# Optimization experiments

Measured on AMD Instinct MI355X. Metric: run time of the kernel, lower is better.

## Reference

```python
import jax, jax.numpy as jnp
import numpy as np

K = 8
TEMP = 0.05
EPS = 1e-8


def setup_inputs() -> dict:
    key = jax.random.key(0)
    k1, k2, k3, k4, k5, k6 = jax.random.split(key, 6)
    N, D, H = 8192, 1024, 64
    h0 = jax.random.normal(k1, (N, D), dtype=jnp.float32)
    coords = jax.random.uniform(k2, (N, 2), dtype=jnp.float32)
    # tiny MLP params: Linear(2,H) -> ReLU -> Linear(H,1) -> Sigmoid
    W1 = jax.random.normal(k3, (2, H), dtype=jnp.float32) * (1.0 / np.sqrt(2))
    b1 = jnp.zeros((H,), dtype=jnp.float32)
    W2 = jax.random.normal(k4, (H, 1), dtype=jnp.float32) * (1.0 / np.sqrt(H))
    b2 = jnp.zeros((1,), dtype=jnp.float32)
    return {"h0": h0, "coords": coords, "W1": W1, "b1": b1, "W2": W2, "b2": b2}


def reference(h0, coords, W1, b1, W2, b2):
    # pairwise euclidean distances [N, N]
    sq = jnp.sum(coords * coords, axis=-1)                      # [N]
    d2 = sq[:, None] + sq[None, :] - 2.0 * (coords @ coords.T)  # [N, N]
    dist = jnp.sqrt(jnp.maximum(d2, 0.0))

    # k+1 nearest (smallest dist), drop self (index 0)
    _, idx = jax.lax.top_k(-dist, K + 1)                        # [N, K+1]
    knn_idx = idx[:, 1:]                                        # [N, K]

    # gather neighbor features [N, K, D]
    neighbor_feats = h0[knn_idx]

    # cosine similarity between h_i and each neighbor (torch eps semantics)
    num = jnp.einsum('nd,nkd->nk', h0, neighbor_feats)          # [N, K]
    ni = jnp.maximum(jnp.linalg.norm(h0, axis=-1), EPS)         # [N]
    nj = jnp.maximum(jnp.linalg.norm(neighbor_feats, axis=-1), EPS)  # [N, K]
    sim = num / (ni[:, None] * nj)

    # spatial weights from gathered distances
    d_knn = jnp.take_along_axis(dist, knn_idx, axis=1)          # [N, K]
    spatial_w = jnp.exp(-d_knn / TEMP)

    density_input = jnp.stack(
        [sim.mean(axis=1), spatial_w.mean(axis=1)], axis=1)     # [N, 2]

    hmid = jax.nn.relu(density_input @ W1 + b1)
    density = jax.nn.sigmoid(hmid @ W2 + b2)                    # [N, 1]
    return density
```

## Files before the change

### kernel.cpp

```cpp
#include <hip/hip_runtime.h>
#include <math.h>

#define NROWS 8192
#define DIM   1024
#define GRID  64
#define CELLW 0.015625f
#define LPR   16

__device__ __forceinline__ int cell_of(float v) {
    int c = (int)(v * 64.0f);
    return c < 0 ? 0 : (c > 63 ? 63 : c);
}

__device__ __forceinline__ float np_d2(float xi, float yi, float sqi,
                                       float xj, float yj) {
    float sqj = __fadd_rn(__fmul_rn(xj, xj), __fmul_rn(yj, yj));
    float G   = fmaf(yi, yj, __fmul_rn(xi, xj));
    return __fsub_rn(__fadd_rn(sqi, sqj), __fmul_rn(2.0f, G));
}

__global__ __launch_bounds__(1024) void build_grid_kernel(
    const float* __restrict__ coords,
    int* __restrict__ cellStart,
    float4* __restrict__ sxyz) {

    __shared__ int lcnt[4096];
    __shared__ int wsum[16];
    const int t = threadIdx.x;

    for (int i = t; i < 4096; i += 1024) lcnt[i] = 0;
    __syncthreads();

    float2 pc[8]; int pcell[8];
#pragma unroll
    for (int k = 0; k < 8; ++k) {
        int i = t + 1024 * k;
        float2 c = ((const float2*)coords)[i];
        pc[k] = c;
        pcell[k] = cell_of(c.y) * GRID + cell_of(c.x);
        atomicAdd(&lcnt[pcell[k]], 1);
    }
    __syncthreads();

    int c0 = lcnt[t*4+0], c1 = lcnt[t*4+1], c2 = lcnt[t*4+2], c3 = lcnt[t*4+3];
    int s1 = c0, s2 = c0 + c1, s3 = s2 + c2, s4 = s3 + c3;
    int lane = t & 63, wid = t >> 6;
    int inc = s4;
#pragma unroll
    for (int off = 1; off < 64; off <<= 1) {
        int o = __shfl_up(inc, off, 64);
        if (lane >= off) inc += o;
    }
    if (lane == 63) wsum[wid] = inc;
    __syncthreads();
    int wbase = 0;
    for (int w = 0; w < wid; ++w) wbase += wsum[w];
    int excl = wbase + inc - s4;

    cellStart[t*4+0] = excl;
    cellStart[t*4+1] = excl + s1;
    cellStart[t*4+2] = excl + s2;
    cellStart[t*4+3] = excl + s3;
    if (t == 1023) cellStart[4096] = excl + s4;
    lcnt[t*4+0] = excl;
    lcnt[t*4+1] = excl + s1;
    lcnt[t*4+2] = excl + s2;
    lcnt[t*4+3] = excl + s3;
    __syncthreads();

#pragma unroll
    for (int k = 0; k < 8; ++k) {
        int pos = atomicAdd(&lcnt[pcell[k]], 1);
        float x = pc[k].x, y = pc[k].y;
        float sq = __fadd_rn(__fmul_rn(x, x), __fmul_rn(y, y));
        sxyz[pos] = make_float4(x, y, sq, __int_as_float(t + 1024 * k));
    }
}

__global__ __launch_bounds__(256) void knn_kernel(
    const int* __restrict__ cellStart,
    const float4* __restrict__ sxyz,
    unsigned long long* __restrict__ chosen_ws) {

    const int sub = threadIdx.x & (LPR - 1);
    const int g   = (blockIdx.x * 256 + threadIdx.x) / LPR;

    const float4 me = sxyz[g];
    const float xi = me.x, yi = me.y, sqi = me.z;
    const int row = __float_as_int(me.w);
    const int cx = cell_of(xi), cy = cell_of(yi);

    unsigned long long best[10], merged[10];
    int C = 2;
    while (true) {
#pragma unroll
        for (int s = 0; s < 10; ++s) best[s] = ~0ULL;
        int x0 = max(0, cx - C), x1 = min(GRID - 1, cx + C);
        int y0 = max(0, cy - C), y1 = min(GRID - 1, cy + C);
        for (int yy = y0; yy <= y1; ++yy) {
            int s = cellStart[yy * GRID + x0];
            int e = cellStart[yy * GRID + x1 + 1];
            for (int t = s + sub; t < e; t += LPR) {
                float4 c = sxyz[t];
                float d2  = __fsub_rn(__fadd_rn(sqi, c.z),
                                      __fmul_rn(2.0f, fmaf(yi, c.y, __fmul_rn(xi, c.x))));
                float dst = __fsqrt_rn(fmaxf(d2, 0.0f));
                unsigned long long key =
                    ((unsigned long long)__float_as_uint(dst) << 32)
                    | (unsigned int)__float_as_int(c.w);
                if (key < best[9]) {
                    best[9] = key;
#pragma unroll
                    for (int ss = 9; ss >= 1; --ss) {
                        unsigned long long a = best[ss - 1], b = best[ss];
                        unsigned long long lo = a < b ? a : b;
                        unsigned long long hi = a < b ? b : a;
                        best[ss - 1] = lo;
                        best[ss]     = hi;
                    }
                }
            }
        }
#pragma unroll
        for (int r = 0; r < 10; ++r) {
            unsigned long long mn = best[0];
#pragma unroll
            for (int off = 1; off < LPR; off <<= 1) {
                unsigned long long o = __shfl_xor(mn, off, 64);
                mn = (o < mn) ? o : mn;
            }
            if (best[0] == mn) {
#pragma unroll
                for (int ss = 0; ss < 9; ++ss) best[ss] = best[ss + 1];
                best[9] = ~0ULL;
            }
            merged[r] = mn;
        }
        bool done = false;
        if (merged[9] != ~0ULL) {
            float d9 = __uint_as_float((unsigned int)(merged[9] >> 32));
            if (d9 + 1.0e-3f <= (float)C * CELLW) done = true;
        }
        if (done || C >= GRID) break;
        C <<= 1; if (C > GRID) C = GRID;
    }

    if (sub == 0) {
        unsigned long long* o = chosen_ws + (size_t)row * 10;
#pragma unroll
        for (int r = 0; r < 10; ++r) o[r] = merged[r];
    }
}

__global__ __launch_bounds__(256) void gather_final_kernel(
    const float* __restrict__ h0,
    const float* __restrict__ coords,
    const unsigned long long* __restrict__ chosen_ws,
    const float4* __restrict__ sxyz,
    const float* __restrict__ W1, const float* __restrict__ b1,
    const float* __restrict__ W2, const float* __restrict__ b2,
    float* __restrict__ out) {

    __shared__ float2 pq[11];

    const int widx = threadIdx.x >> 6;
    const int lane = threadIdx.x & 63;
    const int bid  = blockIdx.x;
    const int g    = (bid & 7) * (NROWS / 8) + (bid >> 3);
    const int row  = __float_as_int(sxyz[g].w);

    const float4* hi = (const float4*)(h0 + (size_t)row * DIM);
    float4 a[4];
#pragma unroll
    for (int t = 0; t < 4; ++t) a[t] = hi[lane + 64 * t];

    const unsigned long long* ch = chosen_ws + (size_t)row * 10;

    for (int s = widx; s <= 10; s += 4) {
        float p = 0.f, q = 0.f;
        if (s == 10) {
#pragma unroll
            for (int t = 0; t < 4; ++t)
                p += a[t].x * a[t].x + a[t].y * a[t].y + a[t].z * a[t].z + a[t].w * a[t].w;
            q = p;
        } else {
            int j = (int)(ch[s] & 0xFFFFFFFFu);
            const float4* hj = (const float4*)(h0 + (size_t)j * DIM);
#pragma unroll
            for (int t = 0; t < 4; ++t) {
                float4 b = hj[lane + 64 * t];
                p += a[t].x * b.x + a[t].y * b.y + a[t].z * b.z + a[t].w * b.w;
                q += b.x * b.x + b.y * b.y + b.z * b.z + b.w * b.w;
            }
        }
#pragma unroll
        for (int off = 1; off < 64; off <<= 1) {
            p += __shfl_xor(p, off, 64);
            q += __shfl_xor(q, off, 64);
        }
        if (lane == 0) pq[s] = make_float2(p, q);
    }
    __syncthreads();

    if (widx != 0) return;

    const float2 ci = ((const float2*)coords)[row];
    const float xi = ci.x, yi = ci.y;
    const float sqi = __fadd_rn(__fmul_rn(xi, xi), __fmul_rn(yi, yi));

    unsigned long long chosen[10];
#pragma unroll
    for (int r = 0; r < 10; ++r) chosen[r] = ch[r];

    auto clamped_d2 = [&](unsigned long long key) -> float {
        int j = (int)(key & 0xFFFFFFFFu);
        float2 cj = ((const float2*)coords)[j];
        return fmaxf(np_d2(xi, yi, sqi, cj.x, cj.y), 0.0f);
    };
    const float m0 = clamped_d2(chosen[0]);
    const float m1 = clamped_d2(chosen[1]);
    const float m2 = clamped_d2(chosen[2]);
    const float m8 = clamped_d2(chosen[8]);
    const float m9 = clamped_d2(chosen[9]);

    const float WIN = 2.0e-6f;
    const bool fpair = (m1 - m0) <= WIN;
    const bool ftri  = fpair && ((m2 - m0) <= WIN);
    const bool f89   = (m9 - m8) <= WIN;

    float wd[3];
    wd[0] = ftri ? (1.f / 3.f) : (fpair ? 0.5f : 1.0f);
    wd[1] = ftri ? (1.f / 3.f) : (fpair ? 0.5f : 0.0f);
    wd[2] = ftri ? (1.f / 3.f) : 0.0f;
    const float wc0 = f89 ? 0.5f : 1.0f;
    const float wc1 = f89 ? 0.5f : 0.0f;

    const float ni = fmaxf(sqrtf(pq[10].x), 1e-8f);

    float sim[10], sw[10];
#pragma unroll
    for (int r = 0; r < 10; ++r) {
        float dst = __uint_as_float((unsigned int)(chosen[r] >> 32));
        float nj  = fmaxf(sqrtf(pq[r].y), 1e-8f);
        sim[r] = pq[r].x / (ni * nj);
        sw[r]  = expf(__fdiv_rn(-dst, 0.05f));
    }

    float Ssim = 0.f, Ssw = 0.f;
#pragma unroll
    for (int r = 0; r < 9; ++r) { Ssim += sim[r]; Ssw += sw[r]; }

    const float w1a = W1[lane], w1b = W1[64 + lane];
    const float b1l = b1[lane], w2l = W2[lane], b2s = b2[0];

    float outacc = 0.f;
#pragma unroll
    for (int d = 0; d < 3; ++d) {
#pragma unroll
        for (int c = 0; c < 2; ++c) {
            float wgt = wd[d] * (c ? wc1 : wc0);
            float simsum = Ssim - sim[d] + (c ? (sim[9] - sim[8]) : 0.f);
            float swsum  = Ssw  - sw[d]  + (c ? (sw[9]  - sw[8])  : 0.f);
            float di0 = simsum * 0.125f;
            float di1 = swsum  * 0.125f;
            float hm = fmaxf(di0 * w1a + di1 * w1b + b1l, 0.f);
            float v  = hm * w2l;
#pragma unroll
            for (int off = 1; off < 64; off <<= 1) v += __shfl_xor(v, off, 64);
            float z = v + b2s;
            outacc += wgt * (1.f / (1.f + expf(-z)));
        }
    }

    if (lane == 0) out[row] = outacc;
}

extern "C" void kernel_launch(void* const* d_in, const int* in_sizes, int n_in,
                              void* d_out, int out_size, void* d_ws, size_t ws_size,
                              hipStream_t stream) {
    const float* h0     = (const float*)d_in[0];
    const float* coords = (const float*)d_in[1];
    const float* W1     = (const float*)d_in[2];
    const float* b1     = (const float*)d_in[3];
    const float* W2     = (const float*)d_in[4];
    const float* b2     = (const float*)d_in[5];
    float* out = (float*)d_out;

    char* ws = (char*)d_ws;
    unsigned long long* chosen_ws = (unsigned long long*)(ws);
    float4* sxyz      = (float4*)(ws + 1015808);
    int*    cellStart = (int*)(ws + 1146880);

    build_grid_kernel  <<<1, 1024, 0, stream>>>(coords, cellStart, sxyz);
    knn_kernel         <<<NROWS * LPR / 256, 256, 0, stream>>>(cellStart, sxyz, chosen_ws);
    gather_final_kernel<<<NROWS, 256, 0, stream>>>(h0, coords, chosen_ws, sxyz,
                                                   W1, b1, W2, b2, out);
}
```

Measured before the change: 63.69 us.

## Map one wavefront per row in gather kernel instead of one block per row

The gather/final kernel now assigns each 64-lane wavefront a whole row, with four rows per 256-thread block, instead of spreading a row's 11 dot products across four waves. Each wave loads the row vector once per chunk and accumulates all ten neighbor dot products and norms in registers. This removes the shared-memory exchange, the __syncthreads, and the three idle waves in the epilogue. The cost is more registers per thread and fewer independent memory streams per row, which may lower occupancy.

Result: faster. 58.37 us (-8.4%).

```diff
diff --git a/kernel.cpp b/kernel.cpp
--- a/kernel.cpp
+++ b/kernel.cpp
@@ -161,56 +161,60 @@
     const float* __restrict__ W2, const float* __restrict__ b2,
     float* __restrict__ out) {
 
-    __shared__ float2 pq[11];
-
-    const int widx = threadIdx.x >> 6;
+    const int wid  = threadIdx.x >> 6;
     const int lane = threadIdx.x & 63;
     const int bid  = blockIdx.x;
-    const int g    = (bid & 7) * (NROWS / 8) + (bid >> 3);
+    const int grp  = (bid & 7) * (gridDim.x / 8) + (bid >> 3);
+    const int g    = grp * 4 + wid;
     const int row  = __float_as_int(sxyz[g].w);
 
+    const unsigned long long* ch = chosen_ws + (size_t)row * 10;
+    unsigned long long chosen[10];
+    int jidx[10];
+#pragma unroll
+    for (int r = 0; r < 10; ++r) {
+        chosen[r] = ch[r];
+        jidx[r]   = (int)(chosen[r] & 0xFFFFFFFFu);
+    }
+
     const float4* hi = (const float4*)(h0 + (size_t)row * DIM);
-    float4 a[4];
-#pragma unroll
-    for (int t = 0; t < 4; ++t) a[t] = hi[lane + 64 * t];
-
-    const unsigned long long* ch = chosen_ws + (size_t)row * 10;
-
-    for (int s = widx; s <= 10; s += 4) {
-        float p = 0.f, q = 0.f;
-        if (s == 10) {
-#pragma unroll
-            for (int t = 0; t < 4; ++t)
-                p += a[t].x * a[t].x + a[t].y * a[t].y + a[t].z * a[t].z + a[t].w * a[t].w;
-            q = p;
-        } else {
-            int j = (int)(ch[s] & 0xFFFFFFFFu);
-            const float4* hj = (const float4*)(h0 + (size_t)j * DIM);
-#pragma unroll
-            for (int t = 0; t < 4; ++t) {
-                float4 b = hj[lane + 64 * t];
-                p += a[t].x * b.x + a[t].y * b.y + a[t].z * b.z + a[t].w * b.w;
-                q += b.x * b.x + b.y * b.y + b.z * b.z + b.w * b.w;
-            }
-        }
-#pragma unroll
-        for (int off = 1; off < 64; off <<= 1) {
-            p += __shfl_xor(p, off, 64);
-            q += __shfl_xor(q, off, 64);
-        }
-        if (lane == 0) pq[s] = make_float2(p, q);
-    }
-    __syncthreads();
-
-    if (widx != 0) return;
+
+    float p[11];
+    float q[10];
+#pragma unroll
+    for (int s = 0; s < 11; ++s) p[s] = 0.f;
+#pragma unroll
+    for (int s = 0; s < 10; ++s) q[s] = 0.f;
+
+    for (int t = 0; t < 4; ++t) {
+        float4 av = hi[lane + 64 * t];
+        p[10] += av.x * av.x + av.y * av.y + av.z * av.z + av.w * av.w;
+#pragma unroll
+        for (int s = 0; s < 10; ++s) {
+            float4 b = ((const float4*)(h0 + (size_t)jidx[s] * DIM))[lane + 64 * t];
+            p[s] += av.x * b.x + av.y * b.y + av.z * b.z + av.w * b.w;
+            q[s] += b.x * b.x + b.y * b.y + b.z * b.z + b.w * b.w;
+        }
+    }
+
+#pragma unroll
+    for (int s = 0; s < 11; ++s) {
+        float v = p[s];
+#pragma unroll
+        for (int off = 1; off < 64; off <<= 1) v += __shfl_xor(v, off, 64);
+        p[s] = v;
+    }
+#pragma unroll
+    for (int s = 0; s < 10; ++s) {
+        float v = q[s];
+#pragma unroll
+        for (int off = 1; off < 64; off <<= 1) v += __shfl_xor(v, off, 64);
+        q[s] = v;
+    }
 
     const float2 ci = ((const float2*)coords)[row];
     const float xi = ci.x, yi = ci.y;
     const float sqi = __fadd_rn(__fmul_rn(xi, xi), __fmul_rn(yi, yi));
-
-    unsigned long long chosen[10];
-#pragma unroll
-    for (int r = 0; r < 10; ++r) chosen[r] = ch[r];
 
     auto clamped_d2 = [&](unsigned long long key) -> float {
         int j = (int)(key & 0xFFFFFFFFu);
@@ -235,14 +239,14 @@
     const float wc0 = f89 ? 0.5f : 1.0f;
     const float wc1 = f89 ? 0.5f : 0.0f;
 
-    const float ni = fmaxf(sqrtf(pq[10].x), 1e-8f);
+    const float ni = fmaxf(sqrtf(p[10]), 1e-8f);
 
     float sim[10], sw[10];
 #pragma unroll
     for (int r = 0; r < 10; ++r) {
         float dst = __uint_as_float((unsigned int)(chosen[r] >> 32));
-        float nj  = fmaxf(sqrtf(pq[r].y), 1e-8f);
-        sim[r] = pq[r].x / (ni * nj);
+        float nj  = fmaxf(sqrtf(q[r]), 1e-8f);
+        sim[r] = p[r] / (ni * nj);
         sw[r]  = expf(__fdiv_rn(-dst, 0.05f));
     }
 
@@ -293,6 +297,6 @@
 
     build_grid_kernel  <<<1, 1024, 0, stream>>>(coords, cellStart, sxyz);
     knn_kernel         <<<NROWS * LPR / 256, 256, 0, stream>>>(cellStart, sxyz, chosen_ws);
-    gather_final_kernel<<<NROWS, 256, 0, stream>>>(h0, coords, chosen_ws, sxyz,
-                                                   W1, b1, W2, b2, out);
-}
+    gather_final_kernel<<<NROWS / 4, 256, 0, stream>>>(h0, coords, chosen_ws, sxyz,
+                                                       W1, b1, W2, b2, out);
+}
```
